# Kernel tuning notes

Measured on AMD Instinct MI355X. Metric: run time of the kernel, lower is better.

Reference implementation:

```python
import jax, jax.numpy as jnp
import numpy as np

HID = 512
HEADS = 8
PF = 2048
EPS = 1e-5


def _layernorm(x, g, b):
    mu = jnp.mean(x, axis=-1, keepdims=True)
    var = jnp.var(x, axis=-1, keepdims=True)
    return (x - mu) * jax.lax.rsqrt(var + EPS) * g + b


def setup_inputs() -> dict:
    key = jax.random.key(0)
    ks = jax.random.split(key, 20)
    s = 0.02
    inp = {
        "trg": jax.random.normal(ks[0], (16, 1024, HID), jnp.float32),
        "src": jax.random.normal(ks[1], (16, 1024, HID), jnp.float32),
        "ln_g": jnp.ones((HID,), jnp.float32),
        "ln_b": jnp.zeros((HID,), jnp.float32),
        "wq": jax.random.normal(ks[2], (HID, HID), jnp.float32) * s,
        "bq": jnp.zeros((HID,), jnp.float32),
        "wk": jax.random.normal(ks[3], (HID, HID), jnp.float32) * s,
        "bk": jnp.zeros((HID,), jnp.float32),
        "wv": jax.random.normal(ks[4], (HID, HID), jnp.float32) * s,
        "bv": jnp.zeros((HID,), jnp.float32),
        "wo": jax.random.normal(ks[5], (HID, HID), jnp.float32) * s,
        "bo": jnp.zeros((HID,), jnp.float32),
        "pf1_w": jax.random.normal(ks[6], (PF, HID), jnp.float32) * s,
        "pf1_b": jnp.zeros((PF,), jnp.float32),
        "pf2_w": jax.random.normal(ks[7], (HID, PF), jnp.float32) * s,
        "pf2_b": jnp.zeros((HID,), jnp.float32),
        "fc1_w": jax.random.normal(ks[8], (256, HID), jnp.float32) * s,
        "fc1_b": jnp.zeros((256,), jnp.float32),
        "fc2_w": jax.random.normal(ks[9], (2, 256), jnp.float32) * s,
        "fc2_b": jnp.zeros((2,), jnp.float32),
    }
    return inp


def reference(trg, src, ln_g, ln_b, wq, bq, wk, bk, wv, bv, wo, bo,
              pf1_w, pf1_b, pf2_w, pf2_b, fc1_w, fc1_b, fc2_w, fc2_b):
    B, T, D = trg.shape
    S = src.shape[1]
    dh = D // HEADS

    # --- multi-head attention (Q=trg, K=V=src, no mask; dropout=eval/no-op) ---
    q = (trg @ wq.T + bq).reshape(B, T, HEADS, dh)
    k = (src @ wk.T + bk).reshape(B, S, HEADS, dh)
    v = (src @ wv.T + bv).reshape(B, S, HEADS, dh)
    scores = jnp.einsum('bqhd,bkhd->bhqk', q, k) / jnp.sqrt(jnp.float32(dh))
    attn = jax.nn.softmax(scores, axis=-1)
    ctx = jnp.einsum('bhqk,bkhd->bqhd', attn, v).reshape(B, T, D)
    sa_out = ctx @ wo.T + bo

    x = _layernorm(trg + sa_out, ln_g, ln_b)

    # --- position-wise feed-forward ---
    h = jax.nn.relu(x @ pf1_w.T + pf1_b)
    ff = h @ pf2_w.T + pf2_b
    x = _layernorm(x + ff, ln_g, ln_b)

    # --- norm-weighted sum pooling over sequence (vectorized) ---
    norm = jnp.linalg.norm(x, axis=2)              # [B, T]
    w = jax.nn.softmax(norm, axis=1)               # [B, T]
    pooled = jnp.einsum('bt,btd->bd', w, x)        # [B, D]

    label = jax.nn.relu(pooled @ fc1_w.T + fc1_b) @ fc2_w.T + fc2_b
    return label
```

## Files before the change

kernel.cpp:

```cpp
#include <hip/hip_runtime.h>

typedef __bf16 bf16x8 __attribute__((ext_vector_type(8)));
typedef float f32x4 __attribute__((ext_vector_type(4)));
typedef unsigned short u16;

__device__ __forceinline__ u16 f2bf(float f){
  unsigned u = __builtin_bit_cast(unsigned, f);
  u += 0x7fffu + ((u>>16)&1u);
  return (u16)(u>>16);
}
__device__ __forceinline__ float bf2f(u16 h){
  unsigned u = ((unsigned)h)<<16; return __builtin_bit_cast(float,u);
}
__device__ __forceinline__ bf16x8 ld8(const u16* p){ return *(const bf16x8*)p; }
__device__ __forceinline__ f32x4 mfma16(bf16x8 a, bf16x8 b, f32x4 c){
  return __builtin_amdgcn_mfma_f32_16x16x32_bf16(a,b,c,0,0,0);
}
__device__ __forceinline__ void gl16(const u16* g, u16* l){
  __builtin_amdgcn_global_load_lds(
    (const __attribute__((address_space(1))) unsigned int*)g,
    (__attribute__((address_space(3))) unsigned int*)l, 16, 0, 0);
}
__device__ __forceinline__ unsigned cvtpk(float a, float b){
  unsigned r;
  asm("v_cvt_pk_bf16_f32 %0, %1, %2" : "=v"(r) : "v"(a), "v"(b));
  return r;
}

#define QSC 0.18033688f

template<int LO>
__global__ __launch_bounds__(256) void k_split(const float* __restrict__ x,
    u16* __restrict__ hi, u16* __restrict__ lo, int n){
  int i = (blockIdx.x*256 + threadIdx.x)*4;
  const int stride = gridDim.x*256*4;
  for(; i<n; i+=stride){
    float4 v = *(const float4*)(x+i);
    u16 h0=f2bf(v.x), h1=f2bf(v.y), h2=f2bf(v.z), h3=f2bf(v.w);
    ushort4 H = {h0,h1,h2,h3};
    *(ushort4*)(hi+i)=H;
    if constexpr(LO){
      ushort4 L = {f2bf(v.x-bf2f(h0)), f2bf(v.y-bf2f(h1)),
                   f2bf(v.z-bf2f(h2)), f2bf(v.w-bf2f(h3))};
      *(ushort4*)(lo+i)=L;
    }
  }
}

template<int EPI, int ALO, int BLO, int BK>
__global__ __launch_bounds__(256) void k_gemm(
  const u16* __restrict__ Ah, const u16* __restrict__ Al,
  const u16* __restrict__ Wh, const u16* __restrict__ Wl,
  const float* __restrict__ bias, int M, int N, int K,
  float* __restrict__ Cf, u16* __restrict__ Oh)
{
  constexpr int SL = BK/8;
  constexpr int SM = SL-1;
  constexpr int RPC = 512/BK;
  __shared__ __align__(16) u16 sAh[128*BK], sWh[128*BK];
  __shared__ __align__(16) u16 sAl[ALO?128*BK:8], sWl[BLO?128*BK:8];
  const int tid = threadIdx.x, w = tid>>6, l = tid&63;
  const int l15 = l&15, g = l>>4;
  const int gx = gridDim.x;
  const int bid = blockIdx.y*gx + blockIdx.x;
  const int nwg = gx*gridDim.y;
  const int wgid = (bid&7)*(nwg>>3) + (bid>>3);
  const int m0 = (wgid/gx)*128, n0 = (wgid%gx)*128;
  const int wr = (w>>1)*64, wc = (w&1)*64;
  f32x4 acc[4][4] = {};
  const int sr = l/SL, sslot = l&SM;
  const int scol = 8*(sslot ^ (sr&SM));
  for(int k0=0;k0<K;k0+=BK){
    #pragma unroll
    for(int i=0;i<BK/16;i++){
      const int rows = w*32 + i*RPC;
      const long ga = (long)(m0+rows+sr)*K + k0 + scol;
      const long gw = (long)(n0+rows+sr)*K + k0 + scol;
      gl16(Ah+ga, sAh + rows*BK);
      gl16(Wh+gw, sWh + rows*BK);
      if constexpr(ALO) gl16(Al+ga, sAl + rows*BK);
      if constexpr(BLO) gl16(Wl+gw, sWl + rows*BK);
    }
    __syncthreads();
    #pragma unroll
    for(int kk=0;kk<BK/32;kk++){
      const int ch8 = 8*((g+4*kk) ^ (l15&SM));
      bf16x8 ah[4], al[4];
      #pragma unroll
      for(int i=0;i<4;i++){
        const int o = (wr + i*16 + l15)*BK + ch8;
        ah[i] = *(const bf16x8*)(sAh + o);
        if constexpr(ALO) al[i] = *(const bf16x8*)(sAl + o);
      }
      #pragma unroll
      for(int j=0;j<4;j++){
        const int o = (wc + j*16 + l15)*BK + ch8;
        bf16x8 bh = *(const bf16x8*)(sWh + o);
        bf16x8 bl;
        if constexpr(BLO) bl = *(const bf16x8*)(sWl + o);
        #pragma unroll
        for(int i=0;i<4;i++){
          acc[i][j] = mfma16(ah[i], bh, acc[i][j]);
          if constexpr(ALO) acc[i][j] = mfma16(al[i], bh, acc[i][j]);
          if constexpr(BLO) acc[i][j] = mfma16(ah[i], bl, acc[i][j]);
        }
      }
    }
    __syncthreads();
  }
  #pragma unroll
  for(int i=0;i<4;i++){
    #pragma unroll
    for(int j=0;j<4;j++){
      const int col  = n0 + wc + j*16 + l15;
      const float bb = bias ? bias[col] : 0.f;
      const int rowb = m0 + wr + i*16 + g*4;
      #pragma unroll
      for(int jj=0;jj<4;jj++){
        float v = acc[i][j][jj] + bb;
        const int row = rowb + jj;
        if constexpr(EPI==0){ Cf[(long)row*N + col] = v; }
        else if constexpr(EPI==1){ Oh[(long)row*N + col] = f2bf(v); }
        else { Oh[(long)row*N + col] = f2bf(fmaxf(v,0.f)); }
      }
    }
  }
}

__global__ __launch_bounds__(256) void k_qkv(
  const u16* __restrict__ trg_hi, const u16* __restrict__ src_hi,
  const u16* __restrict__ Wh,
  const float* __restrict__ bq, const float* __restrict__ bk, const float* __restrict__ bv,
  u16* __restrict__ Qb, u16* __restrict__ Kb, u16* __restrict__ Vt)
{
  __shared__ __align__(16) u16 sAh[128*64], sWh[128*64];
  const int tid = threadIdx.x, w = tid>>6, l = tid&63;
  const int l15 = l&15, g = l>>4;
  const int bid = blockIdx.x;
  const int wgid = (bid&7)*192 + (bid>>3);
  const int m0 = (wgid/12)*128, n0 = (wgid%12)*128;
  const u16* Ah = (n0<512)? trg_hi : src_hi;
  const float* bp = (n0<512)? bq : (n0<1024? bk : bv);
  const int nb = (n0<512)? 0 : (n0<1024? 512 : 1024);
  const int wr = (w>>1)*64, wc = (w&1)*64;
  f32x4 acc[4][4] = {};
  const int sr = l>>3, sslot = l&7;
  const int scol = 8*(sslot ^ (sr&7));
  for(int k0=0;k0<512;k0+=64){
    #pragma unroll
    for(int i=0;i<4;i++){
      const int rows = w*32 + i*8;
      const long ga = (long)(m0+rows+sr)*512 + k0 + scol;
      const long gw = (long)(n0+rows+sr)*512 + k0 + scol;
      gl16(Ah+ga, sAh + rows*64);
      gl16(Wh+gw, sWh + rows*64);
    }
    __syncthreads();
    #pragma unroll
    for(int kk=0;kk<2;kk++){
      const int ch8 = 8*((g+4*kk) ^ (l15&7));
      bf16x8 ah[4];
      #pragma unroll
      for(int i=0;i<4;i++) ah[i] = *(const bf16x8*)(sAh + (wr + i*16 + l15)*64 + ch8);
      #pragma unroll
      for(int j=0;j<4;j++){
        bf16x8 bh = *(const bf16x8*)(sWh + (wc + j*16 + l15)*64 + ch8);
        #pragma unroll
        for(int i=0;i<4;i++){
          acc[i][j] = mfma16(ah[i], bh, acc[i][j]);
        }
      }
    }
    __syncthreads();
  }
  #pragma unroll
  for(int i=0;i<4;i++){
    #pragma unroll
    for(int j=0;j<4;j++){
      const int col = n0 + wc + j*16 + l15;
      const int cl  = col - nb;
      const float bb = bp[cl];
      const int rowb = m0 + wr + i*16 + g*4;
      #pragma unroll
      for(int jj=0;jj<4;jj++){
        float v = acc[i][j][jj] + bb;
        const int row = rowb + jj;
        if(n0 < 512){ Qb[(long)row*512 + cl] = f2bf(v*QSC); }
        else if(n0 < 1024){ Kb[(long)row*512 + cl] = f2bf(v); }
        else {
          const int h = cl>>6, d = cl&63;
          const long dst = (((long)(row>>10)*8 + h)*64 + d)*1024
                         + ((row>>6)&15)*64 + (row&15)*4 + ((row>>4)&3);
          Vt[dst] = f2bf(v);
        }
      }
    }
  }
}

__global__ __launch_bounds__(256) void k_attn(
  const u16* __restrict__ Q, const u16* __restrict__ K,
  const u16* __restrict__ Vt, u16* __restrict__ O)
{
  __shared__ __align__(16) u16 sK[2][64*64], sV[2][64*64];
  __shared__ __align__(16) u16 Ph[4][32*72];
  const int bid = blockIdx.x;
  const int wg = (bid&7)*128 + (bid>>3);
  const int q0 = (wg&7)*128, hd = (wg>>3)&7, b = wg>>6;
  const int tid = threadIdx.x, w = tid>>6, l = tid&63, l15 = l&15, g = l>>4;
  bf16x8 qf[2][2];
  #pragma unroll
  for(int rf=0;rf<2;rf++){
    const int qrow = q0 + rf*64 + w*16 + l15;
    const long qoff = (long)(b*1024 + qrow)*512 + hd*64 + g*8;
    qf[rf][0] = ld8(Q+qoff); qf[rf][1] = ld8(Q+qoff+32);
  }
  const int sr = l>>3, sslot = l&7;
  const int scol = 8*(sslot ^ (sr&7));
  const u16* Kb = K + (long)b*1024*512 + hd*64;
  const u16* Vb = Vt + (long)(b*8+hd)*64*1024;
  f32x4 rs[2] = {};
  f32x4 ctx[2][4] = {};
  #pragma unroll
  for(int i=0;i<2;i++){
    const int rows = w*8 + i*32;
    gl16(Kb + (long)(rows+sr)*512 + scol, sK[0] + rows*64);
    gl16(Vb + (long)(rows+sr)*1024 + scol, sV[0] + rows*64);
  }
  __syncthreads();
  for(int t=0;t<16;t++){
    const int cur = t&1;
    if(t<15){
      const int s1 = (t+1)*64;
      #pragma unroll
      for(int i=0;i<2;i++){
        const int rows = w*8 + i*32;
        gl16(Kb + (long)(s1+rows+sr)*512 + scol, sK[cur^1] + rows*64);
        gl16(Vb + (long)(rows+sr)*1024 + s1 + scol, sV[cur^1] + rows*64);
      }
    }
    #pragma unroll
    for(int rf=0;rf<2;rf++){
      f32x4 sv[4];
      #pragma unroll
      for(int sf=0;sf<4;sf++){
        const int row = sf*16 + l15;
        f32x4 a = {};
        #pragma unroll
        for(int h=0;h<2;h++){
          const int ch = (g + 4*h) ^ (row&7);
          a = mfma16(qf[rf][h], *(const bf16x8*)(sK[cur] + row*64 + ch*8), a);
        }
        sv[sf] = a;
      }
      float p[4][4];
      #pragma unroll
      for(int sf=0;sf<4;sf++){
        #pragma unroll
        for(int j=0;j<4;j++){
          p[sf][j] = exp2f(sv[sf][j]);
          rs[rf][j] += p[sf][j];
        }
      }
      #pragma unroll
      for(int j=0;j<4;j++){
        uint2 pk = { cvtpk(p[0][j], p[1][j]), cvtpk(p[2][j], p[3][j]) };
        *(uint2*)(&Ph[w][(rf*16 + g*4 + j)*72 + l15*4]) = pk;
      }
    }
    #pragma unroll
    for(int ss=0;ss<2;ss++){
      bf16x8 pa0 = *(const bf16x8*)(&Ph[w][(     l15)*72 + ss*32 + g*8]);
      bf16x8 pa1 = *(const bf16x8*)(&Ph[w][(16 + l15)*72 + ss*32 + g*8]);
      #pragma unroll
      for(int df=0;df<4;df++){
        const int row = df*16 + l15;
        const int ch = (ss*4 + g) ^ (row&7);
        const bf16x8 vf = *(const bf16x8*)(sV[cur] + row*64 + ch*8);
        ctx[0][df] = mfma16(pa0, vf, ctx[0][df]);
        ctx[1][df] = mfma16(pa1, vf, ctx[1][df]);
      }
    }
    __syncthreads();
  }
  #pragma unroll
  for(int rf=0;rf<2;rf++){
    float inv[4];
    #pragma unroll
    for(int j=0;j<4;j++){
      float t = rs[rf][j];
      #pragma unroll
      for(int mask=1;mask<16;mask<<=1) t += __shfl_xor(t, mask);
      inv[j] = 1.f/t;
    }
    #pragma unroll
    for(int df=0;df<4;df++){
      #pragma unroll
      for(int j=0;j<4;j++){
        const float v = ctx[rf][df][j] * inv[j];
        const long off = (long)(b*1024 + q0 + rf*64 + w*16 + g*4 + j)*512 + hd*64 + df*16 + l15;
        O[off] = f2bf(v);
      }
    }
  }
}

__global__ __launch_bounds__(256) void k_ln(
  const float* __restrict__ xa, const float* __restrict__ xb,
  const float* __restrict__ gg, const float* __restrict__ bvec,
  float* __restrict__ yf, u16* __restrict__ yh,
  float* __restrict__ norms)
{
  const int w = threadIdx.x>>6, l = threadIdx.x&63;
  const long rrow = (long)blockIdx.x*4 + w;
  const long base = rrow*512 + l*8;
  float4 a0 = *(const float4*)(xa+base), a1 = *(const float4*)(xa+base+4);
  float4 b0 = *(const float4*)(xb+base), b1 = *(const float4*)(xb+base+4);
  float v[8] = {a0.x+b0.x, a0.y+b0.y, a0.z+b0.z, a0.w+b0.w,
                a1.x+b1.x, a1.y+b1.y, a1.z+b1.z, a1.w+b1.w};
  float s=0.f, q=0.f;
  #pragma unroll
  for(int j=0;j<8;j++){ s += v[j]; q += v[j]*v[j]; }
  #pragma unroll
  for(int mask=1;mask<64;mask<<=1){ s += __shfl_xor(s,mask); q += __shfl_xor(q,mask); }
  const float mu  = s*(1.f/512.f);
  const float var = q*(1.f/512.f) - mu*mu;
  const float rstd = rsqrtf(var + 1e-5f);
  float y[8]; float nq = 0.f;
  #pragma unroll
  for(int j=0;j<8;j++){
    const int c = l*8+j;
    y[j] = (v[j]-mu)*rstd*gg[c] + bvec[c];
    nq += y[j]*y[j];
  }
  float4 t0={y[0],y[1],y[2],y[3]}, t1={y[4],y[5],y[6],y[7]};
  *(float4*)(yf+base)=t0; *(float4*)(yf+base+4)=t1;
  if(yh){
    u16 hv[8];
    #pragma unroll
    for(int j=0;j<8;j++){ hv[j]=f2bf(y[j]); }
    ushort4 hh0={hv[0],hv[1],hv[2],hv[3]}, hh1={hv[4],hv[5],hv[6],hv[7]};
    *(ushort4*)(yh+base)=hh0; *(ushort4*)(yh+base+4)=hh1;
  }
  if(norms){
    #pragma unroll
    for(int mask=1;mask<64;mask<<=1) nq += __shfl_xor(nq,mask);
    if(l==0) norms[rrow] = sqrtf(nq);
  }
}

__global__ __launch_bounds__(256) void k_pool2(const float* __restrict__ x2,
   const float* __restrict__ norms, float* __restrict__ partial)
{
  const int b = blockIdx.y, tc = blockIdx.z;
  const int col = blockIdx.x*256 + threadIdx.x;
  __shared__ float wsm[1024];
  __shared__ float red[4];
  const int tid = threadIdx.x, w = tid>>6, l = tid&63;
  float lm = -1e30f;
  for(int i=tid;i<1024;i+=256){ const float n = norms[b*1024+i]; wsm[i]=n; lm=fmaxf(lm,n); }
  #pragma unroll
  for(int mask=1;mask<64;mask<<=1) lm = fmaxf(lm, __shfl_xor(lm,mask));
  __syncthreads();
  if(l==0) red[w]=lm;
  __syncthreads();
  const float bm = fmaxf(fmaxf(red[0],red[1]), fmaxf(red[2],red[3]));
  __syncthreads();
  float ls = 0.f;
  for(int i=tid;i<1024;i+=256){ const float e = __expf(wsm[i]-bm); wsm[i]=e; ls+=e; }
  #pragma unroll
  for(int mask=1;mask<64;mask<<=1) ls += __shfl_xor(ls,mask);
  __syncthreads();
  if(l==0) red[w]=ls;
  __syncthreads();
  const float inv = 1.f/(red[0]+red[1]+red[2]+red[3]);
  float acc = 0.f;
  const int t0 = tc*128;
  for(int t=t0;t<t0+128;t++) acc += wsm[t]*x2[((long)b*1024+t)*512 + col];
  partial[((long)tc*16 + b)*512 + col] = acc*inv;
}

__global__ __launch_bounds__(256) void k_poolr(const float* __restrict__ partial,
   float* __restrict__ pooled)
{
  const int i = blockIdx.x*256 + threadIdx.x;
  float a = 0.f;
  #pragma unroll
  for(int tc=0;tc<8;tc++) a += partial[tc*8192 + i];
  pooled[i] = a;
}

__global__ __launch_bounds__(256) void k_head(const float* __restrict__ pooled,
  const float* __restrict__ w1, const float* __restrict__ b1,
  const float* __restrict__ w2, const float* __restrict__ b2,
  float* __restrict__ out)
{
  __shared__ float ps[16*512];
  __shared__ float h1[16*256];
  const int tid = threadIdx.x;
  for(int i=tid;i<16*512;i+=256) ps[i]=pooled[i];
  __syncthreads();
  float acc[16] = {};
  for(int k=0;k<512;k++){
    const float wv = w1[tid*512+k];
    #pragma unroll
    for(int i=0;i<16;i++) acc[i] += ps[i*512+k]*wv;
  }
  #pragma unroll
  for(int i=0;i<16;i++) h1[i*256+tid] = fmaxf(acc[i]+b1[tid], 0.f);
  __syncthreads();
  if(tid<32){
    const int i = tid>>1, o = tid&1;
    float a = b2[o];
    for(int k=0;k<256;k++) a += h1[i*256+k]*w2[o*256+k];
    out[i*2+o] = a;
  }
}

extern "C" void kernel_launch(void* const* d_in, const int* in_sizes, int n_in,
                              void* d_out, int out_size, void* d_ws, size_t ws_size,
                              hipStream_t stream)
{
  const float* trg  = (const float*)d_in[0];
  const float* src  = (const float*)d_in[1];
  const float* ln_g = (const float*)d_in[2];
  const float* ln_b = (const float*)d_in[3];
  const float* wq   = (const float*)d_in[4];  const float* bq  = (const float*)d_in[5];
  const float* wk   = (const float*)d_in[6];  const float* bk  = (const float*)d_in[7];
  const float* wv   = (const float*)d_in[8];  const float* bv  = (const float*)d_in[9];
  const float* wo   = (const float*)d_in[10]; const float* bo  = (const float*)d_in[11];
  const float* pf1w = (const float*)d_in[12]; const float* pf1b= (const float*)d_in[13];
  const float* pf2w = (const float*)d_in[14]; const float* pf2b= (const float*)d_in[15];
  const float* fc1w = (const float*)d_in[16]; const float* fc1b= (const float*)d_in[17];
  const float* fc2w = (const float*)d_in[18]; const float* fc2b= (const float*)d_in[19];
  float* out = (float*)d_out;

  char* ws = (char*)d_ws;
  const size_t PL = (size_t)16384*512*2;
  auto P = [&](int i)->u16*{ return (u16*)(ws + (size_t)i*PL); };
  u16 *src_hi=P(0), *trg_hi=P(1);
  u16 *Qb=P(2), *Kb=P(3), *Vt=P(4), *ctx=P(5);
  float* sa  = (float*)(ws + 0*PL);
  float* x1f = (float*)(ws + 2*PL);
  u16 *x1_hi = P(4);
  u16 *h_hi  = P(5);
  float* ffb = (float*)(ws + 0*PL);
  float* x2  = (float*)(ws + 5*PL);
  size_t off = 9*PL;
  auto carve = [&](size_t n)->char*{ char* p = ws+off; off += n; return p; };
  u16* wqkv_hi=(u16*)carve((size_t)1536*512*2);
  u16* wo_hi=(u16*)carve(512*512*2);
  u16* p1_hi=(u16*)carve((size_t)2048*512*2);
  u16* p2_hi=(u16*)carve((size_t)512*2048*2);
  float* norms  = (float*)carve(16384*4);
  float* partial= (float*)carve(8*16*512*4);
  float* pooled = (float*)carve(16*512*4);
  (void)ws_size; (void)in_sizes; (void)n_in; (void)out_size;

  const int NTOK = 16384;

  k_split<0><<<dim3(8192),256,0,stream>>>(trg, trg_hi, nullptr, NTOK*512);
  k_split<0><<<dim3(8192),256,0,stream>>>(src, src_hi, nullptr, NTOK*512);
  k_split<0><<<dim3(256),256,0,stream>>>(wq, wqkv_hi,          nullptr, 512*512);
  k_split<0><<<dim3(256),256,0,stream>>>(wk, wqkv_hi+512*512,  nullptr, 512*512);
  k_split<0><<<dim3(256),256,0,stream>>>(wv, wqkv_hi+1024*512, nullptr, 512*512);
  k_split<0><<<dim3(256),256,0,stream>>>(wo, wo_hi, nullptr, 512*512);
  k_split<0><<<dim3(1024),256,0,stream>>>(pf1w, p1_hi, nullptr, 2048*512);
  k_split<0><<<dim3(1024),256,0,stream>>>(pf2w, p2_hi, nullptr, 512*2048);

  k_qkv<<<dim3(1536),256,0,stream>>>(trg_hi,src_hi,wqkv_hi,bq,bk,bv,Qb,Kb,Vt);

  k_attn<<<dim3(1024),256,0,stream>>>(Qb,Kb,Vt,ctx);

  k_gemm<0,0,0,64><<<dim3(4,128),256,0,stream>>>(ctx,nullptr,wo_hi,nullptr,bo,NTOK,512,512,sa,nullptr);
  k_ln<<<dim3(4096),256,0,stream>>>(trg, sa, ln_g, ln_b, x1f, x1_hi, nullptr);

  k_gemm<2,0,0,64><<<dim3(16,128),256,0,stream>>>(x1_hi,nullptr,p1_hi,nullptr,pf1b,NTOK,2048,512,nullptr,h_hi);
  k_gemm<0,0,0,64><<<dim3(4,128),256,0,stream>>>(h_hi,nullptr,p2_hi,nullptr,pf2b,NTOK,512,2048,ffb,nullptr);
  k_ln<<<dim3(4096),256,0,stream>>>(x1f, ffb, ln_g, ln_b, x2, nullptr, norms);

  k_pool2<<<dim3(2,16,8),256,0,stream>>>(x2, norms, partial);
  k_poolr<<<dim3(32),256,0,stream>>>(partial, pooled);
  k_head<<<1,256,0,stream>>>(pooled, fc1w, fc1b, fc2w, fc2b, out);
}
```

Baseline: 354.3 us.

## Double-buffer GEMM LDS tiles with BK=32 and merge split launches

The GEMM and QKV kernels switch from single-buffered BK=64 tiles to double-buffered BK=32 tiles. The next tile is prefetched via global_load_lds while MFMAs run on the current one, which cuts the barriers per tile from two to one and uses a new rotate swizzle with precomputed LDS offsets. The attention loop is unrolled by two with precomputed offsets, and the eight conversion launches are merged into two. Smaller K tiles mean more loop iterations, and the new swizzle may change LDS bank conflicts.

```diff
diff --git a/kernel.cpp b/kernel.cpp
--- a/kernel.cpp
+++ b/kernel.cpp
@@ -29,36 +29,39 @@
 
 #define QSC 0.18033688f
 
-template<int LO>
-__global__ __launch_bounds__(256) void k_split(const float* __restrict__ x,
-    u16* __restrict__ hi, u16* __restrict__ lo, int n){
+__global__ __launch_bounds__(256) void k_split2(const float* __restrict__ a,
+    const float* __restrict__ b, u16* __restrict__ da, u16* __restrict__ db, int n){
+  const float* s = blockIdx.y ? b : a;
+  u16* d = blockIdx.y ? db : da;
   int i = (blockIdx.x*256 + threadIdx.x)*4;
   const int stride = gridDim.x*256*4;
   for(; i<n; i+=stride){
-    float4 v = *(const float4*)(x+i);
-    u16 h0=f2bf(v.x), h1=f2bf(v.y), h2=f2bf(v.z), h3=f2bf(v.w);
-    ushort4 H = {h0,h1,h2,h3};
-    *(ushort4*)(hi+i)=H;
-    if constexpr(LO){
-      ushort4 L = {f2bf(v.x-bf2f(h0)), f2bf(v.y-bf2f(h1)),
-                   f2bf(v.z-bf2f(h2)), f2bf(v.w-bf2f(h3))};
-      *(ushort4*)(lo+i)=L;
-    }
-  }
-}
-
-template<int EPI, int ALO, int BLO, int BK>
+    float4 v = *(const float4*)(s+i);
+    ushort4 H = {f2bf(v.x),f2bf(v.y),f2bf(v.z),f2bf(v.w)};
+    *(ushort4*)(d+i)=H;
+  }
+}
+
+struct SplitW { const float* s[6]; u16* d[6]; int n[6]; };
+__global__ __launch_bounds__(256) void k_splitw(SplitW P){
+  const int y = blockIdx.y;
+  const float* s = P.s[y]; u16* d = P.d[y]; const int n = P.n[y];
+  int i = (blockIdx.x*256 + threadIdx.x)*4;
+  const int stride = gridDim.x*256*4;
+  for(; i<n; i+=stride){
+    float4 v = *(const float4*)(s+i);
+    ushort4 H = {f2bf(v.x),f2bf(v.y),f2bf(v.z),f2bf(v.w)};
+    *(ushort4*)(d+i)=H;
+  }
+}
+
+template<int EPI>
 __global__ __launch_bounds__(256) void k_gemm(
-  const u16* __restrict__ Ah, const u16* __restrict__ Al,
-  const u16* __restrict__ Wh, const u16* __restrict__ Wl,
+  const u16* __restrict__ A, const u16* __restrict__ W,
   const float* __restrict__ bias, int M, int N, int K,
   float* __restrict__ Cf, u16* __restrict__ Oh)
 {
-  constexpr int SL = BK/8;
-  constexpr int SM = SL-1;
-  constexpr int RPC = 512/BK;
-  __shared__ __align__(16) u16 sAh[128*BK], sWh[128*BK];
-  __shared__ __align__(16) u16 sAl[ALO?128*BK:8], sWl[BLO?128*BK:8];
+  __shared__ __align__(16) u16 sA[2][128*32], sW[2][128*32];
   const int tid = threadIdx.x, w = tid>>6, l = tid&63;
   const int l15 = l&15, g = l>>4;
   const int gx = gridDim.x;
@@ -68,46 +71,40 @@
   const int m0 = (wgid/gx)*128, n0 = (wgid%gx)*128;
   const int wr = (w>>1)*64, wc = (w&1)*64;
   f32x4 acc[4][4] = {};
-  const int sr = l/SL, sslot = l&SM;
-  const int scol = 8*(sslot ^ (sr&SM));
-  for(int k0=0;k0<K;k0+=BK){
-    #pragma unroll
-    for(int i=0;i<BK/16;i++){
-      const int rows = w*32 + i*RPC;
-      const long ga = (long)(m0+rows+sr)*K + k0 + scol;
-      const long gw = (long)(n0+rows+sr)*K + k0 + scol;
-      gl16(Ah+ga, sAh + rows*BK);
-      gl16(Wh+gw, sWh + rows*BK);
-      if constexpr(ALO) gl16(Al+ga, sAl + rows*BK);
-      if constexpr(BLO) gl16(Wl+gw, sWl + rows*BK);
-    }
-    __syncthreads();
-    #pragma unroll
-    for(int kk=0;kk<BK/32;kk++){
-      const int ch8 = 8*((g+4*kk) ^ (l15&SM));
-      bf16x8 ah[4], al[4];
-      #pragma unroll
-      for(int i=0;i<4;i++){
-        const int o = (wr + i*16 + l15)*BK + ch8;
-        ah[i] = *(const bf16x8*)(sAh + o);
-        if constexpr(ALO) al[i] = *(const bf16x8*)(sAl + o);
-      }
-      #pragma unroll
-      for(int j=0;j<4;j++){
-        const int o = (wc + j*16 + l15)*BK + ch8;
-        bf16x8 bh = *(const bf16x8*)(sWh + o);
-        bf16x8 bl;
-        if constexpr(BLO) bl = *(const bf16x8*)(sWl + o);
-        #pragma unroll
-        for(int i=0;i<4;i++){
-          acc[i][j] = mfma16(ah[i], bh, acc[i][j]);
-          if constexpr(ALO) acc[i][j] = mfma16(al[i], bh, acc[i][j]);
-          if constexpr(BLO) acc[i][j] = mfma16(ah[i], bl, acc[i][j]);
-        }
-      }
-    }
-    __syncthreads();
-  }
+  const int sr = l>>2, sslot = l&3;
+  const int scol = 8*((sslot - (sr>>1)) & 3);
+  int offA[4], offW[4];
+  #pragma unroll
+  for(int i=0;i<4;i++){ const int R = wr+i*16+l15; offA[i] = R*32 + ((g+(R>>1))&3)*8; }
+  #pragma unroll
+  for(int j=0;j<4;j++){ const int C = wc+j*16+l15; offW[j] = C*32 + ((g+(C>>1))&3)*8; }
+  const u16* Ab = A + (long)m0*K + scol;
+  const u16* Wb = W + (long)n0*K + scol;
+  const int nk = K>>5;
+
+#define G_STAGE(BUF, T) { \
+    const int k0 = (T)<<5; \
+    _Pragma("unroll") \
+    for(int i=0;i<2;i++){ \
+      const int rows = i*64 + w*16; \
+      gl16(Ab + (long)(rows+sr)*K + k0, sA[BUF] + rows*32); \
+      gl16(Wb + (long)(rows+sr)*K + k0, sW[BUF] + rows*32); \
+    } }
+
+#define G_STEP(CUR, T) { \
+    if((T)+1 < nk) G_STAGE(CUR^1, (T)+1); \
+    bf16x8 av[4], wv[4]; \
+    _Pragma("unroll") for(int i=0;i<4;i++) av[i] = *(const bf16x8*)(sA[CUR]+offA[i]); \
+    _Pragma("unroll") for(int j=0;j<4;j++) wv[j] = *(const bf16x8*)(sW[CUR]+offW[j]); \
+    _Pragma("unroll") for(int j=0;j<4;j++){ \
+      _Pragma("unroll") for(int i=0;i<4;i++) acc[i][j] = mfma16(av[i], wv[j], acc[i][j]); } \
+    __syncthreads(); }
+
+  G_STAGE(0,0); __syncthreads();
+  for(int t=0;t<nk;t+=2){ G_STEP(0,t); G_STEP(1,t+1); }
+#undef G_STAGE
+#undef G_STEP
+
   #pragma unroll
   for(int i=0;i<4;i++){
     #pragma unroll
@@ -120,7 +117,6 @@
         float v = acc[i][j][jj] + bb;
         const int row = rowb + jj;
         if constexpr(EPI==0){ Cf[(long)row*N + col] = v; }
-        else if constexpr(EPI==1){ Oh[(long)row*N + col] = f2bf(v); }
         else { Oh[(long)row*N + col] = f2bf(fmaxf(v,0.f)); }
       }
     }
@@ -133,46 +129,50 @@
   const float* __restrict__ bq, const float* __restrict__ bk, const float* __restrict__ bv,
   u16* __restrict__ Qb, u16* __restrict__ Kb, u16* __restrict__ Vt)
 {
-  __shared__ __align__(16) u16 sAh[128*64], sWh[128*64];
+  __shared__ __align__(16) u16 sA[2][128*32], sW[2][128*32];
   const int tid = threadIdx.x, w = tid>>6, l = tid&63;
   const int l15 = l&15, g = l>>4;
   const int bid = blockIdx.x;
   const int wgid = (bid&7)*192 + (bid>>3);
   const int m0 = (wgid/12)*128, n0 = (wgid%12)*128;
-  const u16* Ah = (n0<512)? trg_hi : src_hi;
+  const u16* A = (n0<512)? trg_hi : src_hi;
   const float* bp = (n0<512)? bq : (n0<1024? bk : bv);
   const int nb = (n0<512)? 0 : (n0<1024? 512 : 1024);
   const int wr = (w>>1)*64, wc = (w&1)*64;
   f32x4 acc[4][4] = {};
-  const int sr = l>>3, sslot = l&7;
-  const int scol = 8*(sslot ^ (sr&7));
-  for(int k0=0;k0<512;k0+=64){
-    #pragma unroll
-    for(int i=0;i<4;i++){
-      const int rows = w*32 + i*8;
-      const long ga = (long)(m0+rows+sr)*512 + k0 + scol;
-      const long gw = (long)(n0+rows+sr)*512 + k0 + scol;
-      gl16(Ah+ga, sAh + rows*64);
-      gl16(Wh+gw, sWh + rows*64);
-    }
-    __syncthreads();
-    #pragma unroll
-    for(int kk=0;kk<2;kk++){
-      const int ch8 = 8*((g+4*kk) ^ (l15&7));
-      bf16x8 ah[4];
-      #pragma unroll
-      for(int i=0;i<4;i++) ah[i] = *(const bf16x8*)(sAh + (wr + i*16 + l15)*64 + ch8);
-      #pragma unroll
-      for(int j=0;j<4;j++){
-        bf16x8 bh = *(const bf16x8*)(sWh + (wc + j*16 + l15)*64 + ch8);
-        #pragma unroll
-        for(int i=0;i<4;i++){
-          acc[i][j] = mfma16(ah[i], bh, acc[i][j]);
-        }
-      }
-    }
-    __syncthreads();
-  }
+  const int sr = l>>2, sslot = l&3;
+  const int scol = 8*((sslot - (sr>>1)) & 3);
+  int offA[4], offW[4];
+  #pragma unroll
+  for(int i=0;i<4;i++){ const int R = wr+i*16+l15; offA[i] = R*32 + ((g+(R>>1))&3)*8; }
+  #pragma unroll
+  for(int j=0;j<4;j++){ const int C = wc+j*16+l15; offW[j] = C*32 + ((g+(C>>1))&3)*8; }
+  const u16* Ab = A  + (long)m0*512 + scol;
+  const u16* Wb = Wh + (long)n0*512 + scol;
+
+#define Q_STAGE(BUF, T) { \
+    const int k0 = (T)<<5; \
+    _Pragma("unroll") \
+    for(int i=0;i<2;i++){ \
+      const int rows = i*64 + w*16; \
+      gl16(Ab + (long)(rows+sr)*512 + k0, sA[BUF] + rows*32); \
+      gl16(Wb + (long)(rows+sr)*512 + k0, sW[BUF] + rows*32); \
+    } }
+
+#define Q_STEP(CUR, T) { \
+    if((T)+1 < 16) Q_STAGE(CUR^1, (T)+1); \
+    bf16x8 av[4], wv[4]; \
+    _Pragma("unroll") for(int i=0;i<4;i++) av[i] = *(const bf16x8*)(sA[CUR]+offA[i]); \
+    _Pragma("unroll") for(int j=0;j<4;j++) wv[j] = *(const bf16x8*)(sW[CUR]+offW[j]); \
+    _Pragma("unroll") for(int j=0;j<4;j++){ \
+      _Pragma("unroll") for(int i=0;i<4;i++) acc[i][j] = mfma16(av[i], wv[j], acc[i][j]); } \
+    __syncthreads(); }
+
+  Q_STAGE(0,0); __syncthreads();
+  for(int t=0;t<16;t+=2){ Q_STEP(0,t); Q_STEP(1,t+1); }
+#undef Q_STAGE
+#undef Q_STEP
+
   #pragma unroll
   for(int i=0;i<4;i++){
     #pragma unroll
@@ -219,70 +219,82 @@
   const int scol = 8*(sslot ^ (sr&7));
   const u16* Kb = K + (long)b*1024*512 + hd*64;
   const u16* Vb = Vt + (long)(b*8+hd)*64*1024;
+  int offK[4][2], offV[2][4], offPw[2][4], offPr[2][2];
+  #pragma unroll
+  for(int sf=0;sf<4;sf++){
+    const int row = sf*16 + l15;
+    offK[sf][0] = row*64 + ((g    ^(row&7)))*8;
+    offK[sf][1] = row*64 + (((g+4)^(row&7)))*8;
+  }
+  #pragma unroll
+  for(int ss=0;ss<2;ss++){
+    #pragma unroll
+    for(int df=0;df<4;df++){
+      const int row = df*16 + l15;
+      offV[ss][df] = row*64 + (((ss*4+g)^(row&7)))*8;
+    }
+  }
+  #pragma unroll
+  for(int rf=0;rf<2;rf++){
+    #pragma unroll
+    for(int j=0;j<4;j++) offPw[rf][j] = (rf*16 + g*4 + j)*72 + l15*4;
+    #pragma unroll
+    for(int ss=0;ss<2;ss++) offPr[rf][ss] = (rf*16 + l15)*72 + ss*32 + g*8;
+  }
   f32x4 rs[2] = {};
   f32x4 ctx[2][4] = {};
-  #pragma unroll
-  for(int i=0;i<2;i++){
-    const int rows = w*8 + i*32;
-    gl16(Kb + (long)(rows+sr)*512 + scol, sK[0] + rows*64);
-    gl16(Vb + (long)(rows+sr)*1024 + scol, sV[0] + rows*64);
-  }
-  __syncthreads();
-  for(int t=0;t<16;t++){
-    const int cur = t&1;
-    if(t<15){
-      const int s1 = (t+1)*64;
-      #pragma unroll
-      for(int i=0;i<2;i++){
-        const int rows = w*8 + i*32;
-        gl16(Kb + (long)(s1+rows+sr)*512 + scol, sK[cur^1] + rows*64);
-        gl16(Vb + (long)(rows+sr)*1024 + s1 + scol, sV[cur^1] + rows*64);
-      }
-    }
-    #pragma unroll
-    for(int rf=0;rf<2;rf++){
-      f32x4 sv[4];
-      #pragma unroll
-      for(int sf=0;sf<4;sf++){
-        const int row = sf*16 + l15;
-        f32x4 a = {};
-        #pragma unroll
-        for(int h=0;h<2;h++){
-          const int ch = (g + 4*h) ^ (row&7);
-          a = mfma16(qf[rf][h], *(const bf16x8*)(sK[cur] + row*64 + ch*8), a);
-        }
-        sv[sf] = a;
-      }
-      float p[4][4];
-      #pragma unroll
-      for(int sf=0;sf<4;sf++){
-        #pragma unroll
-        for(int j=0;j<4;j++){
-          p[sf][j] = exp2f(sv[sf][j]);
-          rs[rf][j] += p[sf][j];
-        }
-      }
-      #pragma unroll
-      for(int j=0;j<4;j++){
-        uint2 pk = { cvtpk(p[0][j], p[1][j]), cvtpk(p[2][j], p[3][j]) };
-        *(uint2*)(&Ph[w][(rf*16 + g*4 + j)*72 + l15*4]) = pk;
-      }
-    }
-    #pragma unroll
-    for(int ss=0;ss<2;ss++){
-      bf16x8 pa0 = *(const bf16x8*)(&Ph[w][(     l15)*72 + ss*32 + g*8]);
-      bf16x8 pa1 = *(const bf16x8*)(&Ph[w][(16 + l15)*72 + ss*32 + g*8]);
-      #pragma unroll
-      for(int df=0;df<4;df++){
-        const int row = df*16 + l15;
-        const int ch = (ss*4 + g) ^ (row&7);
-        const bf16x8 vf = *(const bf16x8*)(sV[cur] + row*64 + ch*8);
-        ctx[0][df] = mfma16(pa0, vf, ctx[0][df]);
-        ctx[1][df] = mfma16(pa1, vf, ctx[1][df]);
-      }
-    }
-    __syncthreads();
-  }
+
+#define A_STAGE(BUF, T) { \
+    const long soff = (long)(T)*64; \
+    _Pragma("unroll") \
+    for(int i=0;i<2;i++){ \
+      const int rows = w*8 + i*32; \
+      gl16(Kb + (soff+rows+sr)*512 + scol, sK[BUF] + rows*64); \
+      gl16(Vb + (long)(rows+sr)*1024 + soff + scol, sV[BUF] + rows*64); \
+    } }
+
+#define A_TILE(CUR, T) { \
+    if((T)+1 < 16) A_STAGE(CUR^1, (T)+1); \
+    _Pragma("unroll") \
+    for(int rf=0;rf<2;rf++){ \
+      f32x4 sv[4]; \
+      _Pragma("unroll") \
+      for(int sf=0;sf<4;sf++){ \
+        f32x4 a = {}; \
+        a = mfma16(qf[rf][0], *(const bf16x8*)(sK[CUR]+offK[sf][0]), a); \
+        a = mfma16(qf[rf][1], *(const bf16x8*)(sK[CUR]+offK[sf][1]), a); \
+        sv[sf] = a; \
+      } \
+      float p[4][4]; \
+      _Pragma("unroll") \
+      for(int sf=0;sf<4;sf++){ \
+        _Pragma("unroll") \
+        for(int j=0;j<4;j++){ p[sf][j] = exp2f(sv[sf][j]); rs[rf][j] += p[sf][j]; } \
+      } \
+      _Pragma("unroll") \
+      for(int j=0;j<4;j++){ \
+        uint2 pk = { cvtpk(p[0][j], p[1][j]), cvtpk(p[2][j], p[3][j]) }; \
+        *(uint2*)(&Ph[w][offPw[rf][j]]) = pk; \
+      } \
+    } \
+    _Pragma("unroll") \
+    for(int ss=0;ss<2;ss++){ \
+      bf16x8 pa0 = *(const bf16x8*)(&Ph[w][offPr[0][ss]]); \
+      bf16x8 pa1 = *(const bf16x8*)(&Ph[w][offPr[1][ss]]); \
+      _Pragma("unroll") \
+      for(int df=0;df<4;df++){ \
+        const bf16x8 vf = *(const bf16x8*)(sV[CUR]+offV[ss][df]); \
+        ctx[0][df] = mfma16(pa0, vf, ctx[0][df]); \
+        ctx[1][df] = mfma16(pa1, vf, ctx[1][df]); \
+      } \
+    } \
+    __syncthreads(); }
+
+  A_STAGE(0,0); __syncthreads();
+  for(int t=0;t<16;t+=2){ A_TILE(0,t); A_TILE(1,t+1); }
+#undef A_STAGE
+#undef A_TILE
+
   #pragma unroll
   for(int rf=0;rf<2;rf++){
     float inv[4];
@@ -459,24 +471,25 @@
 
   const int NTOK = 16384;
 
-  k_split<0><<<dim3(8192),256,0,stream>>>(trg, trg_hi, nullptr, NTOK*512);
-  k_split<0><<<dim3(8192),256,0,stream>>>(src, src_hi, nullptr, NTOK*512);
-  k_split<0><<<dim3(256),256,0,stream>>>(wq, wqkv_hi,          nullptr, 512*512);
-  k_split<0><<<dim3(256),256,0,stream>>>(wk, wqkv_hi+512*512,  nullptr, 512*512);
-  k_split<0><<<dim3(256),256,0,stream>>>(wv, wqkv_hi+1024*512, nullptr, 512*512);
-  k_split<0><<<dim3(256),256,0,stream>>>(wo, wo_hi, nullptr, 512*512);
-  k_split<0><<<dim3(1024),256,0,stream>>>(pf1w, p1_hi, nullptr, 2048*512);
-  k_split<0><<<dim3(1024),256,0,stream>>>(pf2w, p2_hi, nullptr, 512*2048);
+  k_split2<<<dim3(8192,2),256,0,stream>>>(trg, src, trg_hi, src_hi, NTOK*512);
+  SplitW sw;
+  sw.s[0]=wq;  sw.d[0]=wqkv_hi;           sw.n[0]=512*512;
+  sw.s[1]=wk;  sw.d[1]=wqkv_hi+512*512;   sw.n[1]=512*512;
+  sw.s[2]=wv;  sw.d[2]=wqkv_hi+1024*512;  sw.n[2]=512*512;
+  sw.s[3]=wo;  sw.d[3]=wo_hi;             sw.n[3]=512*512;
+  sw.s[4]=pf1w; sw.d[4]=p1_hi;            sw.n[4]=2048*512;
+  sw.s[5]=pf2w; sw.d[5]=p2_hi;            sw.n[5]=512*2048;
+  k_splitw<<<dim3(512,6),256,0,stream>>>(sw);
 
   k_qkv<<<dim3(1536),256,0,stream>>>(trg_hi,src_hi,wqkv_hi,bq,bk,bv,Qb,Kb,Vt);
 
   k_attn<<<dim3(1024),256,0,stream>>>(Qb,Kb,Vt,ctx);
 
-  k_gemm<0,0,0,64><<<dim3(4,128),256,0,stream>>>(ctx,nullptr,wo_hi,nullptr,bo,NTOK,512,512,sa,nullptr);
+  k_gemm<0><<<dim3(4,128),256,0,stream>>>(ctx,wo_hi,bo,NTOK,512,512,sa,nullptr);
   k_ln<<<dim3(4096),256,0,stream>>>(trg, sa, ln_g, ln_b, x1f, x1_hi, nullptr);
 
-  k_gemm<2,0,0,64><<<dim3(16,128),256,0,stream>>>(x1_hi,nullptr,p1_hi,nullptr,pf1b,NTOK,2048,512,nullptr,h_hi);
-  k_gemm<0,0,0,64><<<dim3(4,128),256,0,stream>>>(h_hi,nullptr,p2_hi,nullptr,pf2b,NTOK,512,2048,ffb,nullptr);
+  k_gemm<2><<<dim3(16,128),256,0,stream>>>(x1_hi,p1_hi,pf1b,NTOK,2048,512,nullptr,h_hi);
+  k_gemm<0><<<dim3(4,128),256,0,stream>>>(h_hi,p2_hi,pf2b,NTOK,512,2048,ffb,nullptr);
   k_ln<<<dim3(4096),256,0,stream>>>(x1f, ffb, ln_g, ln_b, x2, nullptr, norms);
 
   k_pool2<<<dim3(2,16,8),256,0,stream>>>(x2, norms, partial);
```

Result: no change. 349.0 us (-1.5%).
